# Performance work log

Measured on AMD Instinct MI355X. Metric: run time of the kernel, lower is better.

Reference implementation:

```python
import jax, jax.numpy as jnp
import numpy as np

B, E, D, H = 4096, 16, 512, 2048

def setup_inputs() -> dict:
    key = jax.random.key(0)
    k1, k2, k3, k4 = jax.random.split(key, 4)
    semantic_vec = jax.random.normal(k1, (B, D), dtype=jnp.float32)
    field_centers = jax.random.normal(k2, (E, D), dtype=jnp.float32)
    # Kaiming-uniform-ish Linear init scale
    lim = 1.0 / np.sqrt(D)
    W = jax.random.uniform(k3, (E, H, D), dtype=jnp.float32, minval=-lim, maxval=lim)
    b = jax.random.uniform(k4, (E, H), dtype=jnp.float32, minval=-lim, maxval=lim)
    return {"semantic_vec": semantic_vec, "field_centers": field_centers, "W": W, "b": b}

def reference(semantic_vec, field_centers, W, b):
    # Each expert e: relu((x - c_e) @ W_e^T + b_e); sum over experts.
    # Use linearity: (x - c_e) @ W_e^T = x @ W_e^T - c_e @ W_e^T, avoiding the [B,E,D] offsets tensor.
    xw = jnp.einsum('bd,ehd->beh', semantic_vec, W)          # [B,E,H]
    cw = jnp.einsum('ed,ehd->eh', field_centers, W)          # [E,H]
    pre = xw - cw[None, :, :] + b[None, :, :]                # [B,E,H]
    feature_anchor = jnp.sum(jax.nn.relu(pre), axis=1)       # [B,H]
    return feature_anchor
```

## Files before the change

### kernel.cpp

```cpp
#include <hip/hip_runtime.h>
#include <hip/hip_bf16.h>
#include <stdint.h>
#include <stddef.h>


#define B_DIM 4096
#define E_DIM 16
#define D_DIM 512
#define H_DIM 2048

typedef short bf16x8 __attribute__((ext_vector_type(8)));
typedef float f32x4 __attribute__((ext_vector_type(4)));

__device__ __forceinline__ short f2bf(float f) {
  __hip_bfloat16 h = __float2bfloat16(f);
  return *reinterpret_cast<short*>(&h);
}

__device__ __forceinline__ bf16x8 cvt8(float4 a, float4 b) {
  bf16x8 v;
  v[0] = f2bf(a.x); v[1] = f2bf(a.y); v[2] = f2bf(a.z); v[3] = f2bf(a.w);
  v[4] = f2bf(b.x); v[5] = f2bf(b.y); v[6] = f2bf(b.z); v[7] = f2bf(b.w);
  return v;
}

__device__ __forceinline__ void async_copy16(const void* gptr, void* lptr) {
  __builtin_amdgcn_global_load_lds(
      (const __attribute__((address_space(1))) void*)gptr,
      (__attribute__((address_space(3))) void*)lptr,
      16, 0, 0);
}

__global__ __launch_bounds__(256) void prep(
    const float* __restrict__ W, const float* __restrict__ C,
    const float* __restrict__ bias, const float* __restrict__ X,
    __hip_bfloat16* __restrict__ Wb, float* __restrict__ bias2,
    __hip_bfloat16* __restrict__ Xb) {
  if (blockIdx.x < 8192) {
    const int gw = (blockIdx.x * 256 + threadIdx.x) >> 6;
    const int lane = threadIdx.x & 63;
    const int e = gw >> 11;

    const float* wr = W + (size_t)gw * D_DIM + lane * 8;
    const float* cr = C + (size_t)e * D_DIM + lane * 8;
    float4 w0 = *(const float4*)(wr);
    float4 w1 = *(const float4*)(wr + 4);
    float4 c0 = *(const float4*)(cr);
    float4 c1 = *(const float4*)(cr + 4);

    *(bf16x8*)(Wb + (size_t)gw * D_DIM + lane * 8) = cvt8(w0, w1);

    float dot = w0.x * c0.x + w0.y * c0.y + w0.z * c0.z + w0.w * c0.w +
                w1.x * c1.x + w1.y * c1.y + w1.z * c1.z + w1.w * c1.w;
#pragma unroll
    for (int off = 32; off > 0; off >>= 1) dot += __shfl_down(dot, off, 64);
    if (lane == 0) bias2[gw] = bias[gw] - dot;
  } else {
    const size_t i = ((size_t)(blockIdx.x - 8192) * 256 + threadIdx.x) * 8;
    float4 a = *(const float4*)(X + i);
    float4 b = *(const float4*)(X + i + 4);
    *(bf16x8*)(Xb + i) = cvt8(a, b);
  }
}

__global__ __launch_bounds__(256, 4) void moe_gemm(
    const __hip_bfloat16* __restrict__ Xb,
    const __hip_bfloat16* __restrict__ Wb,
    const float* __restrict__ bias2,
    float* __restrict__ out) {
  __shared__ __align__(16) __hip_bfloat16 As[2][128 * 32];
  __shared__ __align__(16) __hip_bfloat16 Bs[2][2][64 * 32];
  __shared__ __align__(16) float biasS[E_DIM * 64];

  const int tid = threadIdx.x;
  const int lane = tid & 63;
  const int wave = tid >> 6;
  const int hi = blockIdx.x & 31;
  const int mi = blockIdx.x >> 5;
  const int m0 = mi * 128;
  const int h0 = hi * 64;

  for (int idx = tid; idx < E_DIM * 64; idx += 256) {
    biasS[idx] = bias2[((idx >> 6) << 11) + h0 + (idx & 63)];
  }

  const int wm = (wave & 1) * 64;
  const int wn = (wave >> 1) * 32;
  const int lm = lane & 15;
  const int q = lane >> 4;

  const int r = tid >> 2;
  const int fr = (r >> 1) & 3;
  const int col = (((tid & 3) ^ fr)) << 3;
  const size_t aOff0 = (size_t)(m0 + r) * D_DIM + col;
  const size_t aOff1 = (size_t)(m0 + r + 64) * D_DIM + col;
  const size_t bOff = (size_t)(h0 + r) * D_DIM + col;
  const int ldA0 = tid * 8;
  const int ldA1 = (tid + 256) * 8;
  const int ldB = tid * 8;

  int offA[4], offB[2];
#pragma unroll
  for (int i = 0; i < 4; ++i) {
    const int R = wm + i * 16 + lm;
    offA[i] = R * 32 + ((q ^ ((R >> 1) & 3)) << 3);
  }
#pragma unroll
  for (int j = 0; j < 2; ++j) {
    const int R = wn + j * 16 + lm;
    offB[j] = R * 32 + ((q ^ ((R >> 1) & 3)) << 3);
  }

  f32x4 sum[4][2], acc0[4][2], acc1[4][2];
#pragma unroll
  for (int i = 0; i < 4; ++i)
#pragma unroll
    for (int j = 0; j < 2; ++j) {
      sum[i][j] = (f32x4){0.f, 0.f, 0.f, 0.f};
      acc0[i][j] = (f32x4){0.f, 0.f, 0.f, 0.f};
      acc1[i][j] = (f32x4){0.f, 0.f, 0.f, 0.f};
    }

#define STAGE(buf, tt)                                                      \
  {                                                                         \
    const int kk = ((tt) & 15) << 5;                                        \
    const __hip_bfloat16* Bb = Wb + ((size_t)((tt) >> 4) << 21) + bOff + kk;\
    async_copy16(Xb + aOff0 + kk, &As[buf][ldA0]);                          \
    async_copy16(Xb + aOff1 + kk, &As[buf][ldA1]);                          \
    async_copy16(Bb, &Bs[buf][0][ldB]);                                     \
    async_copy16(Bb + ((size_t)1 << 20), &Bs[buf][1][ldB]);                 \
  }

  STAGE(0, 0);
  __syncthreads();

  for (int t = 0; t < 128; ++t) {
    const int cur = t & 1;
    if (t < 127) STAGE(cur ^ 1, t + 1);

    bf16x8 af[4];
#pragma unroll
    for (int i = 0; i < 4; ++i) af[i] = *(const bf16x8*)&As[cur][offA[i]];

#pragma unroll
    for (int j = 0; j < 2; ++j) {
      const bf16x8 b0 = *(const bf16x8*)&Bs[cur][0][offB[j]];
#pragma unroll
      for (int i = 0; i < 4; ++i)
        acc0[i][j] = __builtin_amdgcn_mfma_f32_16x16x32_bf16(
            af[i], b0, acc0[i][j], 0, 0, 0);
      const bf16x8 b1 = *(const bf16x8*)&Bs[cur][1][offB[j]];
#pragma unroll
      for (int i = 0; i < 4; ++i)
        acc1[i][j] = __builtin_amdgcn_mfma_f32_16x16x32_bf16(
            af[i], b1, acc1[i][j], 0, 0, 0);
    }

    if ((t & 15) == 15) {
      const int pair = t >> 4;
#pragma unroll
      for (int j = 0; j < 2; ++j) {
        const float bv0 = biasS[(2 * pair) * 64 + wn + j * 16 + lm];
        const float bv1 = biasS[(2 * pair + 1) * 64 + wn + j * 16 + lm];
#pragma unroll
        for (int i = 0; i < 4; ++i)
#pragma unroll
          for (int u = 0; u < 4; ++u) {
            sum[i][j][u] += fmaxf(acc0[i][j][u] + bv0, 0.f) +
                            fmaxf(acc1[i][j][u] + bv1, 0.f);
            acc0[i][j][u] = 0.f;
            acc1[i][j][u] = 0.f;
          }
      }
    }

    __syncthreads();
  }
#undef STAGE

  const int rbase = q * 4;
#pragma unroll
  for (int i = 0; i < 4; ++i)
#pragma unroll
    for (int j = 0; j < 2; ++j)
#pragma unroll
      for (int u = 0; u < 4; ++u)
        out[(size_t)(m0 + wm + i * 16 + rbase + u) * H_DIM + h0 + wn + j * 16 + lm] =
            sum[i][j][u];
}

__global__ __launch_bounds__(256) void naive_kernel(
    const float* __restrict__ x, const float* __restrict__ c,
    const float* __restrict__ W, const float* __restrict__ bias,
    float* __restrict__ out) {
  const int idx = blockIdx.x * 256 + threadIdx.x;
  const int b = idx >> 11;
  const int h = idx & (H_DIM - 1);
  const float* xr = x + (size_t)b * D_DIM;
  float s = 0.f;
  for (int e = 0; e < E_DIM; ++e) {
    const float* wr = W + ((size_t)e * H_DIM + h) * D_DIM;
    const float* cr = c + (size_t)e * D_DIM;
    float acc = bias[e * H_DIM + h];
    for (int d = 0; d < D_DIM; ++d) acc += (xr[d] - cr[d]) * wr[d];
    s += fmaxf(acc, 0.f);
  }
  out[idx] = s;
}

extern "C" void kernel_launch(void* const* d_in, const int* in_sizes, int n_in,
                              void* d_out, int out_size, void* d_ws, size_t ws_size,
                              hipStream_t stream) {
  const float* x = (const float*)d_in[0];
  const float* c = (const float*)d_in[1];
  const float* W = (const float*)d_in[2];
  const float* b = (const float*)d_in[3];
  float* out = (float*)d_out;

  const size_t sz_wb = (size_t)E_DIM * H_DIM * D_DIM * 2;
  const size_t sz_xb = (size_t)B_DIM * D_DIM * 2;
  const size_t sz_b2 = (size_t)E_DIM * H_DIM * 4;
  const size_t need = sz_wb + sz_xb + sz_b2;

  if (ws_size >= need) {
    __hip_bfloat16* Wb = (__hip_bfloat16*)((char*)d_ws);
    __hip_bfloat16* Xb = (__hip_bfloat16*)((char*)d_ws + sz_wb);
    float* bias2 = (float*)((char*)d_ws + sz_wb + sz_xb);
    prep<<<9216, 256, 0, stream>>>(W, c, b, x, Wb, bias2, Xb);
    moe_gemm<<<1024, 256, 0, stream>>>(Xb, Wb, bias2, out);
  } else {
    naive_kernel<<<(B_DIM * H_DIM) / 256, 256, 0, stream>>>(x, c, W, b, out);
  }
}
```

Baseline: 260.7 us.

## Fuse weight conversion and center-bias into GEMM with larger tiles and triple buffering

Drops the separate prep pass that converted W to bf16 and computed the center-adjusted bias. The GEMM now loads fp32 W directly, converts it to bf16 in registers, writes it to LDS, and accumulates the c·W dot product on the fly. Tiles grow to 256x128 with 512 threads, A gets a three-stage LDS ring, and a block-index swizzle plus explicit waitcnt, barrier and setprio scheduling are added. This removes the bf16 W round-trip through global memory. In exchange, W is now read as fp32 by all 16 M-tiles, which may add L2/HBM traffic and puts the conversion cost inside the GEMM loop.

```diff
diff --git a/kernel.cpp b/kernel.cpp
--- a/kernel.cpp
+++ b/kernel.cpp
@@ -10,6 +10,7 @@
 #define H_DIM 2048
 
 typedef short bf16x8 __attribute__((ext_vector_type(8)));
+typedef short bf16x4 __attribute__((ext_vector_type(4)));
 typedef float f32x4 __attribute__((ext_vector_type(4)));
 
 __device__ __forceinline__ short f2bf(float f) {
@@ -24,6 +25,10 @@
   return v;
 }
 
+__device__ __forceinline__ float dot4(float4 a, float4 b) {
+  return a.x * b.x + a.y * b.y + a.z * b.z + a.w * b.w;
+}
+
 __device__ __forceinline__ void async_copy16(const void* gptr, void* lptr) {
   __builtin_amdgcn_global_load_lds(
       (const __attribute__((address_space(1))) void*)gptr,
@@ -31,162 +36,215 @@
       16, 0, 0);
 }
 
-__global__ __launch_bounds__(256) void prep(
-    const float* __restrict__ W, const float* __restrict__ C,
-    const float* __restrict__ bias, const float* __restrict__ X,
-    __hip_bfloat16* __restrict__ Wb, float* __restrict__ bias2,
-    __hip_bfloat16* __restrict__ Xb) {
-  if (blockIdx.x < 8192) {
-    const int gw = (blockIdx.x * 256 + threadIdx.x) >> 6;
-    const int lane = threadIdx.x & 63;
-    const int e = gw >> 11;
-
-    const float* wr = W + (size_t)gw * D_DIM + lane * 8;
-    const float* cr = C + (size_t)e * D_DIM + lane * 8;
-    float4 w0 = *(const float4*)(wr);
-    float4 w1 = *(const float4*)(wr + 4);
-    float4 c0 = *(const float4*)(cr);
-    float4 c1 = *(const float4*)(cr + 4);
-
-    *(bf16x8*)(Wb + (size_t)gw * D_DIM + lane * 8) = cvt8(w0, w1);
-
-    float dot = w0.x * c0.x + w0.y * c0.y + w0.z * c0.z + w0.w * c0.w +
-                w1.x * c1.x + w1.y * c1.y + w1.z * c1.z + w1.w * c1.w;
-#pragma unroll
-    for (int off = 32; off > 0; off >>= 1) dot += __shfl_down(dot, off, 64);
-    if (lane == 0) bias2[gw] = bias[gw] - dot;
-  } else {
-    const size_t i = ((size_t)(blockIdx.x - 8192) * 256 + threadIdx.x) * 8;
-    float4 a = *(const float4*)(X + i);
-    float4 b = *(const float4*)(X + i + 4);
-    *(bf16x8*)(Xb + i) = cvt8(a, b);
-  }
-}
-
-__global__ __launch_bounds__(256, 4) void moe_gemm(
+__global__ __launch_bounds__(256) void prep_x(
+    const float* __restrict__ X, __hip_bfloat16* __restrict__ Xb) {
+  const size_t t = (size_t)blockIdx.x * 256 + threadIdx.x;
+  const size_t i0 = t * 8;
+  float4 a0 = *(const float4*)(X + i0);
+  float4 a1 = *(const float4*)(X + i0 + 4);
+  *(bf16x8*)(Xb + i0) = cvt8(a0, a1);
+}
+
+__global__ __launch_bounds__(512, 2) void moe_gemm9(
     const __hip_bfloat16* __restrict__ Xb,
-    const __hip_bfloat16* __restrict__ Wb,
-    const float* __restrict__ bias2,
+    const float* __restrict__ W,
+    const float* __restrict__ C,
+    const float* __restrict__ bias,
     float* __restrict__ out) {
-  __shared__ __align__(16) __hip_bfloat16 As[2][128 * 32];
-  __shared__ __align__(16) __hip_bfloat16 Bs[2][2][64 * 32];
-  __shared__ __align__(16) float biasS[E_DIM * 64];
+  __shared__ __align__(16) char smem[156160];
 
   const int tid = threadIdx.x;
   const int lane = tid & 63;
   const int wave = tid >> 6;
-  const int hi = blockIdx.x & 31;
-  const int mi = blockIdx.x >> 5;
-  const int m0 = mi * 128;
-  const int h0 = hi * 64;
-
-  for (int idx = tid; idx < E_DIM * 64; idx += 256) {
-    biasS[idx] = bias2[((idx >> 6) << 11) + h0 + (idx & 63)];
-  }
-
-  const int wm = (wave & 1) * 64;
-  const int wn = (wave >> 1) * 32;
+
+  const int swz = (blockIdx.x & 7) * 32 + (blockIdx.x >> 3);
+  const int hi = swz >> 4;
+  const int mi = swz & 15;
+  const int m0 = mi * 256;
+  const int h0 = hi * 128;
+
+  const int wm = (wave >> 1) * 64;
+  const int wn = (wave & 1) * 64;
   const int lm = lane & 15;
   const int q = lane >> 4;
 
-  const int r = tid >> 2;
-  const int fr = (r >> 1) & 3;
-  const int col = (((tid & 3) ^ fr)) << 3;
-  const size_t aOff0 = (size_t)(m0 + r) * D_DIM + col;
-  const size_t aOff1 = (size_t)(m0 + r + 64) * D_DIM + col;
-  const size_t bOff = (size_t)(h0 + r) * D_DIM + col;
-  const int ldA0 = tid * 8;
-  const int ldA1 = (tid + 256) * 8;
-  const int ldB = tid * 8;
-
-  int offA[4], offB[2];
-#pragma unroll
-  for (int i = 0; i < 4; ++i) {
-    const int R = wm + i * 16 + lm;
-    offA[i] = R * 32 + ((q ^ ((R >> 1) & 3)) << 3);
-  }
+  int aSrc[4];
+#pragma unroll
+  for (int j = 0; j < 4; ++j) {
+    const int n = j * 512 + tid;
+    const int r = n >> 3;
+    const int c = (n & 7) ^ (r & 7);
+    aSrc[j] = r * D_DIM + c * 8;
+  }
+
+  const int rB0 = tid >> 3;
+  int wOffE[2], oB[2];
 #pragma unroll
   for (int j = 0; j < 2; ++j) {
-    const int R = wn + j * 16 + lm;
-    offB[j] = R * 32 + ((q ^ ((R >> 1) & 3)) << 3);
-  }
-
-  f32x4 sum[4][2], acc0[4][2], acc1[4][2];
-#pragma unroll
-  for (int i = 0; i < 4; ++i)
-#pragma unroll
-    for (int j = 0; j < 2; ++j) {
-      sum[i][j] = (f32x4){0.f, 0.f, 0.f, 0.f};
-      acc0[i][j] = (f32x4){0.f, 0.f, 0.f, 0.f};
-      acc1[i][j] = (f32x4){0.f, 0.f, 0.f, 0.f};
-    }
-
-#define STAGE(buf, tt)                                                      \
-  {                                                                         \
-    const int kk = ((tt) & 15) << 5;                                        \
-    const __hip_bfloat16* Bb = Wb + ((size_t)((tt) >> 4) << 21) + bOff + kk;\
-    async_copy16(Xb + aOff0 + kk, &As[buf][ldA0]);                          \
-    async_copy16(Xb + aOff1 + kk, &As[buf][ldA1]);                          \
-    async_copy16(Bb, &Bs[buf][0][ldB]);                                     \
-    async_copy16(Bb + ((size_t)1 << 20), &Bs[buf][1][ldB]);                 \
-  }
-
-  STAGE(0, 0);
-  __syncthreads();
-
-  for (int t = 0; t < 128; ++t) {
-    const int cur = t & 1;
-    if (t < 127) STAGE(cur ^ 1, t + 1);
-
-    bf16x8 af[4];
-#pragma unroll
-    for (int i = 0; i < 4; ++i) af[i] = *(const bf16x8*)&As[cur][offA[i]];
-
-#pragma unroll
-    for (int j = 0; j < 2; ++j) {
-      const bf16x8 b0 = *(const bf16x8*)&Bs[cur][0][offB[j]];
-#pragma unroll
-      for (int i = 0; i < 4; ++i)
-        acc0[i][j] = __builtin_amdgcn_mfma_f32_16x16x32_bf16(
-            af[i], b0, acc0[i][j], 0, 0, 0);
-      const bf16x8 b1 = *(const bf16x8*)&Bs[cur][1][offB[j]];
-#pragma unroll
-      for (int i = 0; i < 4; ++i)
-        acc1[i][j] = __builtin_amdgcn_mfma_f32_16x16x32_bf16(
-            af[i], b1, acc1[i][j], 0, 0, 0);
-    }
-
-    if ((t & 15) == 15) {
-      const int pair = t >> 4;
-#pragma unroll
-      for (int j = 0; j < 2; ++j) {
-        const float bv0 = biasS[(2 * pair) * 64 + wn + j * 16 + lm];
-        const float bv1 = biasS[(2 * pair + 1) * 64 + wn + j * 16 + lm];
-#pragma unroll
-        for (int i = 0; i < 4; ++i)
+    const int n = j * 512 + tid;
+    const int r = n >> 3;
+    const int c = (n & 7) ^ (r & 7);
+    oB[j] = c * 8;
+    wOffE[j] = r * D_DIM + c * 8;
+  }
+
+  int aRd[4][2], bRd[4][2];
+#pragma unroll
+  for (int m = 0; m < 4; ++m) {
+    const int R = wm + m * 16 + lm;
+#pragma unroll
+    for (int s = 0; s < 2; ++s)
+      aRd[m][s] = R * 128 + (((s * 4 + q) ^ (R & 7)) << 4);
+  }
+#pragma unroll
+  for (int n = 0; n < 4; ++n) {
+    const int R = wn + n * 16 + lm;
+#pragma unroll
+    for (int s = 0; s < 2; ++s)
+      bRd[n][s] = 32768 + R * 128 + (((s * 4 + q) ^ (R & 7)) << 4);
+  }
+
+  float* biasS = (float*)(smem + 147456);
+  float* cwF = (float*)(smem + 155648);
+
+#define STAGEA(bufOff, gg)                                                   \
+  {                                                                          \
+    const int k0 = ((gg) & 7) << 6;                                          \
+    const __hip_bfloat16* Ag = Xb + (size_t)m0 * D_DIM + k0;                 \
+    _Pragma("unroll")                                                        \
+    for (int j = 0; j < 4; ++j)                                              \
+      async_copy16(Ag + aSrc[j], smem + (bufOff) + (j * 512 + tid) * 16);    \
+  }
+
+#define LOADB(gg)                                                            \
+  {                                                                          \
+    const int k0 = ((gg) & 7) << 6;                                          \
+    const float* Wg =                                                        \
+        W + ((size_t)((gg) >> 3) << 20) + (size_t)h0 * D_DIM + k0;           \
+    const float* Cg = C + (((gg) >> 3) << 9) + k0;                           \
+    wA0 = *(const float4*)(Wg + wOffE[0]);                                   \
+    wA1 = *(const float4*)(Wg + wOffE[0] + 4);                               \
+    wB0 = *(const float4*)(Wg + wOffE[1]);                                   \
+    wB1 = *(const float4*)(Wg + wOffE[1] + 4);                               \
+    cA0 = *(const float4*)(Cg + oB[0]);                                      \
+    cA1 = *(const float4*)(Cg + oB[0] + 4);                                  \
+    cB0 = *(const float4*)(Cg + oB[1]);                                      \
+    cB1 = *(const float4*)(Cg + oB[1] + 4);                                  \
+  }
+
+#define PROCB(bufOff)                                                        \
+  {                                                                          \
+    *(bf16x8*)(smem + (bufOff) + 32768 + tid * 16) = cvt8(wA0, wA1);         \
+    *(bf16x8*)(smem + (bufOff) + 32768 + (512 + tid) * 16) = cvt8(wB0, wB1); \
+    part0 += dot4(wA0, cA0) + dot4(wA1, cA1);                                \
+    part1 += dot4(wB0, cB0) + dot4(wB1, cB1);                                \
+  }
+
+  float4 wA0, wA1, wB0, wB1, cA0, cA1, cB0, cB1;
+  float part0 = 0.f, part1 = 0.f;
+
+  STAGEA(0, 0);
+  STAGEA(49152, 1);
+  LOADB(0);
+#pragma unroll
+  for (int j = 0; j < 4; ++j) {
+    const int idx = j * 512 + tid;
+    biasS[idx] = bias[((idx >> 7) << 11) + h0 + (idx & 127)];
+  }
+  PROCB(0);
+  asm volatile("s_waitcnt lgkmcnt(0)" ::: "memory");
+  __builtin_amdgcn_s_barrier();
+  __builtin_amdgcn_sched_barrier(0);
+
+  f32x4 sum[4][4], acc[4][4];
+#pragma unroll
+  for (int m = 0; m < 4; ++m)
+#pragma unroll
+    for (int n = 0; n < 4; ++n) {
+      sum[m][n] = (f32x4){0.f, 0.f, 0.f, 0.f};
+      acc[m][n] = (f32x4){0.f, 0.f, 0.f, 0.f};
+    }
+
+  int bC = 0, bN = 49152, bS2 = 98304;
+
+  for (int g = 0; g < 128; ++g) {
+    if (g < 127) LOADB(g + 1);
+    if (g < 126) STAGEA(bS2, g + 2);
+
+#pragma unroll
+    for (int s = 0; s < 2; ++s) {
+      bf16x8 aF[4], bF[4];
+#pragma unroll
+      for (int m = 0; m < 4; ++m)
+        aF[m] = *(const bf16x8*)(smem + bC + aRd[m][s]);
+#pragma unroll
+      for (int n = 0; n < 4; ++n)
+        bF[n] = *(const bf16x8*)(smem + bC + bRd[n][s]);
+      asm volatile("s_waitcnt lgkmcnt(0)" ::: "memory");
+      __builtin_amdgcn_sched_barrier(0);
+      __builtin_amdgcn_s_setprio(1);
+#pragma unroll
+      for (int m = 0; m < 4; ++m)
+#pragma unroll
+        for (int n = 0; n < 4; ++n)
+          acc[m][n] = __builtin_amdgcn_mfma_f32_16x16x32_bf16(
+              aF[m], bF[n], acc[m][n], 0, 0, 0);
+      __builtin_amdgcn_s_setprio(0);
+    }
+
+    if ((g & 7) == 7) {
+      const float* bS = biasS + ((g >> 3) << 7);
+#pragma unroll
+      for (int n = 0; n < 4; ++n) {
+        const int col = wn + n * 16 + lm;
+        const float bvn = bS[col] - cwF[col];
+#pragma unroll
+        for (int m = 0; m < 4; ++m)
 #pragma unroll
           for (int u = 0; u < 4; ++u) {
-            sum[i][j][u] += fmaxf(acc0[i][j][u] + bv0, 0.f) +
-                            fmaxf(acc1[i][j][u] + bv1, 0.f);
-            acc0[i][j][u] = 0.f;
-            acc1[i][j][u] = 0.f;
+            sum[m][n][u] += fmaxf(acc[m][n][u] + bvn, 0.f);
+            acc[m][n][u] = 0.f;
           }
       }
     }
 
-    __syncthreads();
-  }
-#undef STAGE
-
-  const int rbase = q * 4;
-#pragma unroll
-  for (int i = 0; i < 4; ++i)
-#pragma unroll
-    for (int j = 0; j < 2; ++j)
+    if (g < 127) {
+      PROCB(bN);
+      if (((g + 1) & 7) == 7) {
+        float p0 = part0, p1 = part1;
+        p0 += __shfl_xor(p0, 1, 64);
+        p0 += __shfl_xor(p0, 2, 64);
+        p0 += __shfl_xor(p0, 4, 64);
+        p1 += __shfl_xor(p1, 1, 64);
+        p1 += __shfl_xor(p1, 2, 64);
+        p1 += __shfl_xor(p1, 4, 64);
+        if ((lane & 7) == 0) {
+          cwF[rB0] = p0;
+          cwF[64 + rB0] = p1;
+        }
+        part0 = 0.f;
+        part1 = 0.f;
+      }
+    }
+
+    asm volatile("s_waitcnt vmcnt(4) lgkmcnt(0)" ::: "memory");
+    __builtin_amdgcn_s_barrier();
+    __builtin_amdgcn_sched_barrier(0);
+
+    const int t_ = bC; bC = bN; bN = bS2; bS2 = t_;
+  }
+#undef STAGEA
+#undef LOADB
+#undef PROCB
+
+#pragma unroll
+  for (int m = 0; m < 4; ++m)
+#pragma unroll
+    for (int n = 0; n < 4; ++n)
 #pragma unroll
       for (int u = 0; u < 4; ++u)
-        out[(size_t)(m0 + wm + i * 16 + rbase + u) * H_DIM + h0 + wn + j * 16 + lm] =
-            sum[i][j][u];
+        out[(size_t)(m0 + wm + m * 16 + q * 4 + u) * H_DIM +
+            h0 + wn + n * 16 + lm] = sum[m][n][u];
 }
 
 __global__ __launch_bounds__(256) void naive_kernel(
@@ -217,17 +275,12 @@
   const float* b = (const float*)d_in[3];
   float* out = (float*)d_out;
 
-  const size_t sz_wb = (size_t)E_DIM * H_DIM * D_DIM * 2;
   const size_t sz_xb = (size_t)B_DIM * D_DIM * 2;
-  const size_t sz_b2 = (size_t)E_DIM * H_DIM * 4;
-  const size_t need = sz_wb + sz_xb + sz_b2;
-
-  if (ws_size >= need) {
-    __hip_bfloat16* Wb = (__hip_bfloat16*)((char*)d_ws);
-    __hip_bfloat16* Xb = (__hip_bfloat16*)((char*)d_ws + sz_wb);
-    float* bias2 = (float*)((char*)d_ws + sz_wb + sz_xb);
-    prep<<<9216, 256, 0, stream>>>(W, c, b, x, Wb, bias2, Xb);
-    moe_gemm<<<1024, 256, 0, stream>>>(Xb, Wb, bias2, out);
+
+  if (ws_size >= sz_xb) {
+    __hip_bfloat16* Xb = (__hip_bfloat16*)d_ws;
+    prep_x<<<1024, 256, 0, stream>>>(x, Xb);
+    moe_gemm9<<<256, 512, 0, stream>>>(Xb, W, c, b, out);
   } else {
     naive_kernel<<<(B_DIM * H_DIM) / 256, 256, 0, stream>>>(x, c, W, b, out);
   }
```

After: 293.2 us. 1.12x slower.
